# Performance work log

Hardware: AMD Instinct MI355X
Metric: run time of the kernel (lower is better)

The kernel has to match this reference:

```python
import jax, jax.numpy as jnp
import numpy as np

B, H, W, C = 32, 56, 56, 512
NH, WS, SS = 16, 7, 3
HD = C // NH
N = WS * WS
HID = int(C * 4.0)
SCALE = HD ** -0.5
EPS = 1e-5


def _window_partition(x):
    # x: (B, H, W, C) -> (B*nW, WS, WS, C)
    b = x.shape[0]
    x = x.reshape(b, H // WS, WS, W // WS, WS, C)
    return x.transpose(0, 1, 3, 2, 4, 5).reshape(-1, WS, WS, C)


def _window_reverse(wins):
    b = wins.shape[0] // ((H // WS) * (W // WS))
    x = wins.reshape(b, H // WS, W // WS, WS, WS, C)
    return x.transpose(0, 1, 3, 2, 4, 5).reshape(b, H, W, C)


def _ln(x, g, b):
    mu = jnp.mean(x, -1, keepdims=True)
    var = jnp.mean((x - mu) ** 2, -1, keepdims=True)
    return (x - mu) * jax.lax.rsqrt(var + EPS) * g + b


def setup_inputs():
    key = jax.random.key(0)
    ks = jax.random.split(key, 8)

    def w(k, shape, s=0.02):
        return jax.random.normal(k, shape, jnp.float32) * s

    # relative position index (static, same recipe as Swin)
    coords = np.stack(np.meshgrid(np.arange(WS), np.arange(WS), indexing='ij'))  # (2,WS,WS)
    cf = coords.reshape(2, -1)
    rel = (cf[:, :, None] - cf[:, None, :]).transpose(1, 2, 0).astype(np.int64)
    rel[:, :, 0] += WS - 1
    rel[:, :, 1] += WS - 1
    rel[:, :, 0] *= 2 * WS - 1
    rel_index = jnp.asarray(rel.sum(-1), jnp.int32)  # (N, N)

    # shifted-window attention mask (static)
    img = np.zeros((H, W), np.float32)
    cnt = 0
    for hs in (slice(0, -WS), slice(-WS, -SS), slice(-SS, None)):
        for vs in (slice(0, -WS), slice(-WS, -SS), slice(-SS, None)):
            img[hs, vs] = cnt
            cnt += 1
    mw = img.reshape(H // WS, WS, W // WS, WS).transpose(0, 2, 1, 3).reshape(-1, N)
    am = mw[:, None, :] - mw[:, :, None]
    attn_mask = jnp.asarray(np.where(am != 0, -100.0, 0.0).astype(np.float32))  # (nW, N, N)

    return {
        'x': jax.random.normal(ks[0], (B, H * W, C), jnp.float32),
        'norm1_g': jnp.ones((C,), jnp.float32), 'norm1_b': jnp.zeros((C,), jnp.float32),
        'qkv_w': w(ks[1], (C, 3 * C)), 'qkv_b': jnp.zeros((3 * C,), jnp.float32),
        'rel_bias_table': w(ks[2], ((2 * WS - 1) ** 2, NH)),
        'proj_w': w(ks[3], (C, C)), 'proj_b': jnp.zeros((C,), jnp.float32),
        'norm2_g': jnp.ones((C,), jnp.float32), 'norm2_b': jnp.zeros((C,), jnp.float32),
        'fc1_w': w(ks[4], (C, HID)), 'fc1_b': jnp.zeros((HID,), jnp.float32),
        'fc2_w': w(ks[5], (HID, C)), 'fc2_b': jnp.zeros((C,), jnp.float32),
        'rel_index': rel_index,
        'attn_mask': attn_mask,
    }


def reference(x, norm1_g, norm1_b, qkv_w, qkv_b, rel_bias_table, proj_w, proj_b,
              norm2_g, norm2_b, fc1_w, fc1_b, fc2_w, fc2_b, rel_index, attn_mask):
    shortcut = x
    h = _ln(x, norm1_g, norm1_b).reshape(B, H, W, C)
    # cyclic shift (shift_size > 0 -> SW-MSA)
    h = jnp.roll(h, shift=(-SS, -SS), axis=(1, 2))
    wins = _window_partition(h).reshape(-1, N, C)  # (B*nW, N, C)
    Bn = wins.shape[0]

    qkv = (wins @ qkv_w + qkv_b).reshape(Bn, N, 3, NH, HD).transpose(2, 0, 3, 1, 4)
    q, k, v = qkv[0] * SCALE, qkv[1], qkv[2]  # (Bn, NH, N, HD)
    attn = jnp.einsum('bhnd,bhmd->bhnm', q, k)  # (Bn, NH, N, N)

    bias = rel_bias_table[rel_index.reshape(-1)].reshape(N, N, NH).transpose(2, 0, 1)
    attn = attn + bias[None]

    nW = attn_mask.shape[0]
    attn = attn.reshape(Bn // nW, nW, NH, N, N) + attn_mask[None, :, None]
    attn = jax.nn.softmax(attn.reshape(Bn, NH, N, N), axis=-1)

    o = jnp.einsum('bhnm,bhmd->bhnd', attn, v).transpose(0, 2, 1, 3).reshape(Bn, N, C)
    o = o @ proj_w + proj_b

    h = _window_reverse(o.reshape(-1, WS, WS, C))
    h = jnp.roll(h, shift=(SS, SS), axis=(1, 2)).reshape(B, H * W, C)
    x = shortcut + h

    m = _ln(x, norm2_g, norm2_b)
    m = jax.nn.gelu(m @ fc1_w + fc1_b, approximate=False) @ fc2_w + fc2_b
    return x + m
```

## Files before the change

kernel.cpp:

```cpp
#include <hip/hip_runtime.h>
#include <hip/hip_bf16.h>


typedef unsigned short u16;
typedef __bf16 bf16x8 __attribute__((ext_vector_type(8)));
typedef float floatx4 __attribute__((ext_vector_type(4)));

#define MROWS 100352
#define SCALE_ATTN 0.17677669529663687f

__device__ __forceinline__ float b2f(u16 u) {
    union { unsigned int i; float f; } c; c.i = ((unsigned int)u) << 16; return c.f;
}
__device__ __forceinline__ u16 f2b(float f) {
    union { float f; unsigned int u; } c; c.f = f;
    unsigned int r = c.u + 0x7fffu + ((c.u >> 16) & 1u);
    return (u16)(r >> 16);
}

__device__ __forceinline__ int win_token(int win, int n) {
    int b  = win >> 6;
    int wi = (win & 63) >> 3;
    int wj = win & 7;
    int ti = n / 7;
    int tj = n - ti * 7;
    int ii = wi * 7 + ti + 3; if (ii >= 56) ii -= 56;
    int jj = wj * 7 + tj + 3; if (jj >= 56) jj -= 56;
    return b * 3136 + ii * 56 + jj;
}

__global__ void detect_flag(const unsigned int* __restrict__ g1, int* __restrict__ flag) {
    if (threadIdx.x == 0 && blockIdx.x == 0)
        *flag = (g1[0] == 0x3F800000u) ? 1 : 0;
}

__global__ __launch_bounds__(256)
void conv_f32(const void* __restrict__ src, float* __restrict__ dst, int n,
              const int* __restrict__ flag) {
    int i = blockIdx.x * 256 + threadIdx.x;
    if (i >= n) return;
    if (*flag) dst[i] = ((const float*)src)[i];
    else       dst[i] = b2f(((const u16*)src)[i]);
}

__global__ __launch_bounds__(256)
void transpose_k(const void* __restrict__ srcv, u16* __restrict__ dst, int R, int Cc,
                 const int* __restrict__ flag) {
    const bool f32 = (*flag != 0);
    __shared__ u16 tile[32][33];
    int tx = threadIdx.x & 31, ty = threadIdx.x >> 5;
    int c0 = blockIdx.x << 5, r0 = blockIdx.y << 5;
#pragma unroll
    for (int j = 0; j < 4; ++j) {
        size_t idx = (size_t)(r0 + ty + j * 8) * Cc + c0 + tx;
        tile[ty + j * 8][tx] = f32 ? f2b(((const float*)srcv)[idx]) : ((const u16*)srcv)[idx];
    }
    __syncthreads();
#pragma unroll
    for (int j = 0; j < 4; ++j)
        dst[(size_t)(c0 + ty + j * 8) * R + r0 + tx] = tile[tx][ty + j * 8];
}

__global__ __launch_bounds__(256)
void bias_expand(const float* __restrict__ tblf, const int* __restrict__ ridx,
                 float* __restrict__ biasf) {
    int i = blockIdx.x * 256 + threadIdx.x;
    if (i < 16 * 2401) {
        int head = i / 2401, r = i - head * 2401;
        biasf[i] = tblf[ridx[r] * 16 + head];
    }
}

template <bool REMAP>
__global__ __launch_bounds__(256)
void ln_kernel(const void* __restrict__ srcv, const float* __restrict__ g,
               const float* __restrict__ bb, u16* __restrict__ dst,
               const int* __restrict__ flag) {
    int row = blockIdx.x;
    size_t srow;
    if (REMAP) {
        int win = row / 49, n = row - win * 49;
        srow = (size_t)win_token(win, n);
    } else {
        srow = (size_t)row;
    }
    int t = threadIdx.x;
    float v0, v1;
    if (REMAP && *flag) {
        float2 u = *(const float2*)((const float*)srcv + srow * 512 + t * 2);
        v0 = u.x; v1 = u.y;
    } else {
        ushort2 u = *(const ushort2*)((const u16*)srcv + srow * 512 + t * 2);
        v0 = b2f(u.x); v1 = b2f(u.y);
    }
    float sum = v0 + v1, sq = v0 * v0 + v1 * v1;
#pragma unroll
    for (int off = 32; off > 0; off >>= 1) {
        sum += __shfl_down(sum, off);
        sq  += __shfl_down(sq, off);
    }
    __shared__ float s1[4], s2[4];
    int wv = t >> 6, ln = t & 63;
    if (ln == 0) { s1[wv] = sum; s2[wv] = sq; }
    __syncthreads();
    float tot  = s1[0] + s1[1] + s1[2] + s1[3];
    float tot2 = s2[0] + s2[1] + s2[2] + s2[3];
    float mean = tot * (1.0f / 512.0f);
    float var  = tot2 * (1.0f / 512.0f) - mean * mean;
    float rstd = rsqrtf(var + 1e-5f);
    float o0 = (v0 - mean) * rstd * g[t * 2]     + bb[t * 2];
    float o1 = (v1 - mean) * rstd * g[t * 2 + 1] + bb[t * 2 + 1];
    ushort2 ou; ou.x = f2b(o0); ou.y = f2b(o1);
    *(ushort2*)(dst + (size_t)row * 512 + t * 2) = ou;
}

template <int MODE>
__global__ __launch_bounds__(256)
void gemm128(const u16* __restrict__ A, const u16* __restrict__ Bt,
             const float* __restrict__ bias, int K, int Nn,
             void* __restrict__ outv, const void* __restrict__ resv,
             const int* __restrict__ flag, int row_off) {
    __shared__ __align__(16) u16 As[128 * 40];
    __shared__ __align__(16) u16 Bs[128 * 40];
    const int tid = threadIdx.x;
    const int bm = blockIdx.x, bn = blockIdx.y;
    const int wave = tid >> 6, lane = tid & 63;
    const int wr = (wave >> 1) << 6, wc = (wave & 1) << 6;
    const int lm = lane & 15, lq = lane >> 4;
    const bool f32 = (*flag != 0);

    floatx4 acc[4][4];
#pragma unroll
    for (int i = 0; i < 4; ++i)
#pragma unroll
        for (int j = 0; j < 4; ++j)
            acc[i][j] = (floatx4){0.f, 0.f, 0.f, 0.f};

    const size_t arow0 = (size_t)bm * 128;
    const size_t brow0 = (size_t)bn * 128;

    for (int k0 = 0; k0 < K; k0 += 32) {
#pragma unroll
        for (int it = 0; it < 2; ++it) {
            int chunk = tid + (it << 8);
            int r = chunk >> 2;
            int kc = (chunk & 3) << 3;
            uint4 da = *(const uint4*)(A  + (arow0 + r) * K + k0 + kc);
            uint4 db = *(const uint4*)(Bt + (brow0 + r) * K + k0 + kc);
            *(uint4*)(&As[r * 40 + kc]) = da;
            *(uint4*)(&Bs[r * 40 + kc]) = db;
        }
        __syncthreads();
        bf16x8 af[4], bf[4];
#pragma unroll
        for (int i = 0; i < 4; ++i)
            af[i] = *(const bf16x8*)(&As[(wr + (i << 4) + lm) * 40 + (lq << 3)]);
#pragma unroll
        for (int j = 0; j < 4; ++j)
            bf[j] = *(const bf16x8*)(&Bs[(wc + (j << 4) + lm) * 40 + (lq << 3)]);
#pragma unroll
        for (int i = 0; i < 4; ++i)
#pragma unroll
            for (int j = 0; j < 4; ++j)
                acc[i][j] = __builtin_amdgcn_mfma_f32_16x16x32_bf16(af[i], bf[j], acc[i][j], 0, 0, 0);
        __syncthreads();
    }

#pragma unroll
    for (int i = 0; i < 4; ++i) {
#pragma unroll
        for (int r = 0; r < 4; ++r) {
            const int row = (bm << 7) + wr + (i << 4) + (lq << 2) + r;
            size_t orow;
            if (MODE == 2) {
                int win = row / 49, n = row - win * 49;
                orow = (size_t)win_token(win, n);
            } else {
                orow = (size_t)row;
            }
#pragma unroll
            for (int j = 0; j < 4; ++j) {
                const int col = (bn << 7) + wc + (j << 4) + lm;
                float v = acc[i][j][r] + bias[col];
                if (MODE == 0) {
                    ((u16*)outv)[(size_t)row * Nn + col] = f2b(v);
                } else if (MODE == 1) {
                    v = 0.5f * v * (1.0f + erff(v * 0.70710678118654752f));
                    ((u16*)outv)[(size_t)row * Nn + col] = f2b(v);
                } else if (MODE == 2) {
                    float res = f32 ? ((const float*)resv)[orow * 512 + col]
                                    : b2f(((const u16*)resv)[orow * 512 + col]);
                    ((u16*)outv)[orow * 512 + col] = f2b(v + res);
                } else {
                    float res = b2f(((const u16*)resv)[(size_t)row * Nn + col]);
                    size_t grow = (size_t)(row + row_off);
                    if (f32) ((float*)outv)[grow * Nn + col] = v + res;
                    else     ((u16*)outv)[grow * Nn + col]  = f2b(v + res);
                }
            }
        }
    }
}

__global__ __launch_bounds__(64)
void attn_kernel(const u16* __restrict__ qkv, const float* __restrict__ biasf,
                 const float* __restrict__ amaskf, u16* __restrict__ o, int win_base) {
    const int blk = blockIdx.x;
    const int winl = blk >> 4, head = blk & 15;
    const int wing = win_base + winl;
    const int w = wing & 63;
    const int t = threadIdx.x;
    __shared__ float qf[49 * 32], kf[49 * 32], vf[49 * 32];
    const size_t base = (size_t)winl * 49 * 1536 + head * 32;
    for (int idx = t; idx < 392; idx += 64) {
        int m = idx >> 3, d = (idx & 7) << 2;
        size_t rb = base + (size_t)m * 1536 + d;
        ushort4 uq = *(const ushort4*)(qkv + rb);
        ushort4 uk = *(const ushort4*)(qkv + rb + 512);
        ushort4 uv = *(const ushort4*)(qkv + rb + 1024);
        int o4 = m * 32 + d;
        qf[o4 + 0] = b2f(uq.x); qf[o4 + 1] = b2f(uq.y);
        qf[o4 + 2] = b2f(uq.z); qf[o4 + 3] = b2f(uq.w);
        kf[o4 + 0] = b2f(uk.x); kf[o4 + 1] = b2f(uk.y);
        kf[o4 + 2] = b2f(uk.z); kf[o4 + 3] = b2f(uk.w);
        vf[o4 + 0] = b2f(uv.x); vf[o4 + 1] = b2f(uv.y);
        vf[o4 + 2] = b2f(uv.z); vf[o4 + 3] = b2f(uv.w);
    }
    __syncthreads();
    if (t < 49) {
        float q[32];
#pragma unroll
        for (int d = 0; d < 32; ++d) q[d] = qf[t * 32 + d] * SCALE_ATTN;
        float s[49];
        float mx = -1e30f;
        const float* bp = biasf + head * 2401 + t * 49;
        const float* mp = amaskf + w * 2401 + t * 49;
#pragma unroll
        for (int m = 0; m < 49; ++m) {
            float acc = 0.f;
#pragma unroll
            for (int d = 0; d < 32; ++d) acc += q[d] * kf[m * 32 + d];
            acc += bp[m] + mp[m];
            s[m] = acc;
            mx = fmaxf(mx, acc);
        }
        float sum = 0.f;
#pragma unroll
        for (int m = 0; m < 49; ++m) { s[m] = __expf(s[m] - mx); sum += s[m]; }
        float inv = 1.0f / sum;
        float ov[32];
#pragma unroll
        for (int d = 0; d < 32; ++d) ov[d] = 0.f;
#pragma unroll
        for (int m = 0; m < 49; ++m) {
            float p = s[m];
#pragma unroll
            for (int d = 0; d < 32; ++d) ov[d] += p * vf[m * 32 + d];
        }
        u16* op = o + (size_t)(wing * 49 + t) * 512 + head * 32;
#pragma unroll
        for (int dc = 0; dc < 32; dc += 4) {
            ushort4 pk;
            pk.x = f2b(ov[dc + 0] * inv); pk.y = f2b(ov[dc + 1] * inv);
            pk.z = f2b(ov[dc + 2] * inv); pk.w = f2b(ov[dc + 3] * inv);
            *(ushort4*)(op + dc) = pk;
        }
    }
}

extern "C" void kernel_launch(void* const* d_in, const int* in_sizes, int n_in,
                              void* d_out, int out_size, void* d_ws, size_t ws_size,
                              hipStream_t stream) {
    const void* x      = d_in[0];
    const void* n1g    = d_in[1];
    const void* n1b    = d_in[2];
    const void* qkv_w  = d_in[3];
    const void* qkv_b  = d_in[4];
    const void* relt   = d_in[5];
    const void* proj_w = d_in[6];
    const void* proj_b = d_in[7];
    const void* n2g    = d_in[8];
    const void* n2b    = d_in[9];
    const void* fc1_w  = d_in[10];
    const void* fc1_b  = d_in[11];
    const void* fc2_w  = d_in[12];
    const void* fc2_b  = d_in[13];
    const int*  ridx   = (const int*)d_in[14];
    const void* amask  = d_in[15];

    char* ws = (char*)d_ws;
    u16*  wT_qkv  = (u16*)(ws);
    u16*  wT_proj = (u16*)(ws + 1572864);
    u16*  wT_fc1  = (u16*)(ws + 2097152);
    u16*  wT_fc2  = (u16*)(ws + 4194304);
    float* biasf  = (float*)(ws + 6291456);
    float* amaskf = (float*)(ws + 6445120);
    float* qkv_bf = (float*)(ws + 7059776);
    float* proj_bf= (float*)(ws + 7065920);
    float* fc1_bf = (float*)(ws + 7067968);
    float* fc2_bf = (float*)(ws + 7076160);
    float* n1gf   = (float*)(ws + 7078208);
    float* n1bf   = (float*)(ws + 7080256);
    float* n2gf   = (float*)(ws + 7082304);
    float* n2bf   = (float*)(ws + 7084352);
    float* reltf  = (float*)(ws + 7086400);
    int*   flag   = (int*)(ws + 7097216);
    u16* bufA = (u16*)(ws + 8388608);
    u16* bufB = (u16*)(ws + 8388608 + 102760448);
    u16* bufC = (u16*)(ws + 8388608 + 102760448 + 77070336);

    detect_flag<<<1, 64, 0, stream>>>((const unsigned int*)n1g, flag);

    conv_f32<<<6, 256, 0, stream>>>(qkv_b, qkv_bf, 1536, flag);
    conv_f32<<<2, 256, 0, stream>>>(proj_b, proj_bf, 512, flag);
    conv_f32<<<8, 256, 0, stream>>>(fc1_b, fc1_bf, 2048, flag);
    conv_f32<<<2, 256, 0, stream>>>(fc2_b, fc2_bf, 512, flag);
    conv_f32<<<2, 256, 0, stream>>>(n1g, n1gf, 512, flag);
    conv_f32<<<2, 256, 0, stream>>>(n1b, n1bf, 512, flag);
    conv_f32<<<2, 256, 0, stream>>>(n2g, n2gf, 512, flag);
    conv_f32<<<2, 256, 0, stream>>>(n2b, n2bf, 512, flag);
    conv_f32<<<11, 256, 0, stream>>>(relt, reltf, 169 * 16, flag);
    conv_f32<<<(64 * 2401 + 255) / 256, 256, 0, stream>>>(amask, amaskf, 64 * 2401, flag);

    transpose_k<<<dim3(48, 16), 256, 0, stream>>>(qkv_w, wT_qkv, 512, 1536, flag);
    transpose_k<<<dim3(16, 16), 256, 0, stream>>>(proj_w, wT_proj, 512, 512, flag);
    transpose_k<<<dim3(64, 16), 256, 0, stream>>>(fc1_w, wT_fc1, 512, 2048, flag);
    transpose_k<<<dim3(16, 64), 256, 0, stream>>>(fc2_w, wT_fc2, 2048, 512, flag);
    bias_expand<<<(16 * 2401 + 255) / 256, 256, 0, stream>>>(reltf, ridx, biasf);

    ln_kernel<true><<<MROWS, 256, 0, stream>>>(x, n1gf, n1bf, bufA, flag);

    for (int c = 0; c < 4; ++c) {
        const u16* Ain = bufA + (size_t)c * 25088 * 512;
        gemm128<0><<<dim3(196, 12), 256, 0, stream>>>(Ain, wT_qkv, qkv_bf, 512, 1536, bufB, nullptr, flag, 0);
        attn_kernel<<<512 * 16, 64, 0, stream>>>(bufB, biasf, amaskf, bufC, c * 512);
    }

    gemm128<2><<<dim3(784, 4), 256, 0, stream>>>(bufC, wT_proj, proj_bf, 512, 512, bufA, x, flag, 0);

    ln_kernel<false><<<MROWS, 256, 0, stream>>>(bufA, n2gf, n2bf, bufC, flag);

    for (int mc0 = 0; mc0 < MROWS; mc0 += 16384) {
        int rows = (MROWS - mc0 < 16384) ? (MROWS - mc0) : 16384;
        int tiles = rows >> 7;
        gemm128<1><<<dim3(tiles, 16), 256, 0, stream>>>(bufC + (size_t)mc0 * 512, wT_fc1, fc1_bf, 512, 2048, bufB, nullptr, flag, 0);
        gemm128<3><<<dim3(tiles, 4), 256, 0, stream>>>(bufB, wT_fc2, fc2_bf, 2048, 512, d_out, bufA + (size_t)mc0 * 512, flag, mc0);
    }
}
```

Baseline: 2.418 ms.

## Rewrite GEMM as 256x256 tile with async global-to-LDS double buffering

Replaces the 128x128 register-staged GEMM with a 256x256, 512-thread kernel. It loads tiles directly into LDS via global_load_lds, double-buffered with explicit waitcnt/barrier pipelining, uses an XOR-swizzled LDS layout, and remaps workgroups across XCDs. The aim is to hide global load latency, cut LDS bank conflicts and raise data reuse per tile for all four GEMMs. The trade-off is much higher register and LDS pressure, plus tight reliance on hand-placed wait counts for correctness. Row counts must also divide evenly by 256.

```diff
diff --git a/kernel.cpp b/kernel.cpp
--- a/kernel.cpp
+++ b/kernel.cpp
@@ -28,6 +28,11 @@
     int jj = wj * 7 + tj + 3; if (jj >= 56) jj -= 56;
     return b * 3136 + ii * 56 + jj;
 }
+
+#define GL2LDS(gaddr, laddr) \
+    __builtin_amdgcn_global_load_lds((const __attribute__((address_space(1))) void*)(gaddr), \
+                                     (__attribute__((address_space(3))) void*)(laddr), 16, 0, 0)
+#define SCHED0() __builtin_amdgcn_sched_barrier(0)
 
 __global__ void detect_flag(const unsigned int* __restrict__ g1, int* __restrict__ flag) {
     if (threadIdx.x == 0 && blockIdx.x == 0)
@@ -115,62 +120,113 @@
 }
 
 template <int MODE>
-__global__ __launch_bounds__(256)
-void gemm128(const u16* __restrict__ A, const u16* __restrict__ Bt,
-             const float* __restrict__ bias, int K, int Nn,
+__global__ __launch_bounds__(512, 2)
+void gemm256(const u16* __restrict__ A, const u16* __restrict__ Bt,
+             const float* __restrict__ bias, int K, int Nn, int nbn,
              void* __restrict__ outv, const void* __restrict__ resv,
              const int* __restrict__ flag, int row_off) {
-    __shared__ __align__(16) u16 As[128 * 40];
-    __shared__ __align__(16) u16 Bs[128 * 40];
+    __shared__ __align__(16) u16 As[2 * 16384];
+    __shared__ __align__(16) u16 Bs[2 * 16384];
     const int tid = threadIdx.x;
-    const int bm = blockIdx.x, bn = blockIdx.y;
+
+    const int nwg = (int)gridDim.x;
+    const int bid = (int)blockIdx.x;
+    const int q8 = nwg >> 3, r8 = nwg & 7;
+    const int xcd = bid & 7, sidx = bid >> 3;
+    const int xb = (xcd < r8) ? xcd * (q8 + 1) : r8 * (q8 + 1) + (xcd - r8) * q8;
+    const int wg = xb + sidx;
+    const int bm = wg / nbn, bn = wg - bm * nbn;
+
     const int wave = tid >> 6, lane = tid & 63;
-    const int wr = (wave >> 1) << 6, wc = (wave & 1) << 6;
+    const int wm = wave >> 2, wn = wave & 3;
     const int lm = lane & 15, lq = lane >> 4;
-    const bool f32 = (*flag != 0);
-
-    floatx4 acc[4][4];
-#pragma unroll
-    for (int i = 0; i < 4; ++i)
+    const int lm7 = lm & 7;
+
+    floatx4 acc[8][4];
+#pragma unroll
+    for (int i = 0; i < 8; ++i)
 #pragma unroll
         for (int j = 0; j < 4; ++j)
             acc[i][j] = (floatx4){0.f, 0.f, 0.f, 0.f};
 
-    const size_t arow0 = (size_t)bm * 128;
-    const size_t brow0 = (size_t)bn * 128;
-
-    for (int k0 = 0; k0 < K; k0 += 32) {
-#pragma unroll
-        for (int it = 0; it < 2; ++it) {
-            int chunk = tid + (it << 8);
-            int r = chunk >> 2;
-            int kc = (chunk & 3) << 3;
-            uint4 da = *(const uint4*)(A  + (arow0 + r) * K + k0 + kc);
-            uint4 db = *(const uint4*)(Bt + (brow0 + r) * K + k0 + kc);
-            *(uint4*)(&As[r * 40 + kc]) = da;
-            *(uint4*)(&Bs[r * 40 + kc]) = db;
+    const size_t arow0 = (size_t)bm * 256;
+    const size_t brow0 = (size_t)bn * 256;
+
+    const int crow = lane >> 3;
+    const int csl  = ((lane & 7) ^ crow) << 3;
+    const u16* gA[4]; const u16* gB[4]; int lofs[4];
+#pragma unroll
+    for (int qq = 0; qq < 4; ++qq) {
+        const int c = (wave << 2) + qq;
+        gA[qq] = A  + (arow0 + c * 8 + crow) * (size_t)K + csl;
+        gB[qq] = Bt + (brow0 + c * 8 + crow) * (size_t)K + csl;
+        lofs[qq] = c << 9;
+    }
+    const int NT = K >> 6;
+
+    auto STAGE = [&](int buf, int kt) {
+        const size_t ko = (size_t)kt << 6;
+        const int lb_ = buf << 14;
+#pragma unroll
+        for (int qq = 0; qq < 4; ++qq) {
+            GL2LDS(gA[qq] + ko, &As[lb_ + lofs[qq]]);
+            GL2LDS(gB[qq] + ko, &Bs[lb_ + lofs[qq]]);
         }
-        __syncthreads();
-        bf16x8 af[4], bf[4];
-#pragma unroll
-        for (int i = 0; i < 4; ++i)
-            af[i] = *(const bf16x8*)(&As[(wr + (i << 4) + lm) * 40 + (lq << 3)]);
+    };
+
+    STAGE(0, 0);
+    STAGE(1, 1);
+    SCHED0();
+    asm volatile("s_waitcnt vmcnt(8)" ::: "memory");
+    SCHED0();
+    __builtin_amdgcn_s_barrier();
+    SCHED0();
+
+    for (int t = 0; t < NT; ++t) {
+        const int lb = (t & 1) << 14;
+        bf16x8 af[8], bfv[4];
+#pragma unroll
+        for (int i = 0; i < 8; ++i)
+            af[i] = *(const bf16x8*)(&As[lb + ((wm << 7) + (i << 4) + lm) * 64 + ((lq ^ lm7) << 3)]);
 #pragma unroll
         for (int j = 0; j < 4; ++j)
-            bf[j] = *(const bf16x8*)(&Bs[(wc + (j << 4) + lm) * 40 + (lq << 3)]);
-#pragma unroll
-        for (int i = 0; i < 4; ++i)
+            bfv[j] = *(const bf16x8*)(&Bs[lb + ((wn << 6) + (j << 4) + lm) * 64 + ((lq ^ lm7) << 3)]);
+#pragma unroll
+        for (int i = 0; i < 8; ++i)
 #pragma unroll
             for (int j = 0; j < 4; ++j)
-                acc[i][j] = __builtin_amdgcn_mfma_f32_16x16x32_bf16(af[i], bf[j], acc[i][j], 0, 0, 0);
-        __syncthreads();
-    }
-
-#pragma unroll
-    for (int i = 0; i < 4; ++i) {
-#pragma unroll
-        for (int r = 0; r < 4; ++r) {
-            const int row = (bm << 7) + wr + (i << 4) + (lq << 2) + r;
+                acc[i][j] = __builtin_amdgcn_mfma_f32_16x16x32_bf16(af[i], bfv[j], acc[i][j], 0, 0, 0);
+#pragma unroll
+        for (int i = 0; i < 8; ++i)
+            af[i] = *(const bf16x8*)(&As[lb + ((wm << 7) + (i << 4) + lm) * 64 + (((4 + lq) ^ lm7) << 3)]);
+#pragma unroll
+        for (int j = 0; j < 4; ++j)
+            bfv[j] = *(const bf16x8*)(&Bs[lb + ((wn << 6) + (j << 4) + lm) * 64 + (((4 + lq) ^ lm7) << 3)]);
+        asm volatile("s_waitcnt lgkmcnt(0)" ::: "memory");
+        SCHED0();
+        __builtin_amdgcn_s_barrier();
+        SCHED0();
+        if (t + 2 < NT) STAGE(t & 1, t + 2);
+        SCHED0();
+#pragma unroll
+        for (int i = 0; i < 8; ++i)
+#pragma unroll
+            for (int j = 0; j < 4; ++j)
+                acc[i][j] = __builtin_amdgcn_mfma_f32_16x16x32_bf16(af[i], bfv[j], acc[i][j], 0, 0, 0);
+        SCHED0();
+        if (t + 2 < NT) asm volatile("s_waitcnt vmcnt(8)" ::: "memory");
+        else            asm volatile("s_waitcnt vmcnt(0)" ::: "memory");
+        SCHED0();
+        __builtin_amdgcn_s_barrier();
+        SCHED0();
+    }
+
+    const bool f32 = (MODE >= 2) ? (*flag != 0) : false;
+#pragma unroll
+    for (int i = 0; i < 8; ++i) {
+#pragma unroll
+        for (int rr = 0; rr < 4; ++rr) {
+            const int row = (bm << 8) + (wm << 7) + (i << 4) + (lq << 2) + rr;
             size_t orow;
             if (MODE == 2) {
                 int win = row / 49, n = row - win * 49;
@@ -180,8 +236,8 @@
             }
 #pragma unroll
             for (int j = 0; j < 4; ++j) {
-                const int col = (bn << 7) + wc + (j << 4) + lm;
-                float v = acc[i][j][r] + bias[col];
+                const int col = (bn << 8) + (wn << 6) + (j << 4) + lm;
+                float v = acc[i][j][rr] + bias[col];
                 if (MODE == 0) {
                     ((u16*)outv)[(size_t)row * Nn + col] = f2b(v);
                 } else if (MODE == 1) {
@@ -332,18 +388,18 @@
 
     for (int c = 0; c < 4; ++c) {
         const u16* Ain = bufA + (size_t)c * 25088 * 512;
-        gemm128<0><<<dim3(196, 12), 256, 0, stream>>>(Ain, wT_qkv, qkv_bf, 512, 1536, bufB, nullptr, flag, 0);
+        gemm256<0><<<98 * 6, 512, 0, stream>>>(Ain, wT_qkv, qkv_bf, 512, 1536, 6, bufB, nullptr, flag, 0);
         attn_kernel<<<512 * 16, 64, 0, stream>>>(bufB, biasf, amaskf, bufC, c * 512);
     }
 
-    gemm128<2><<<dim3(784, 4), 256, 0, stream>>>(bufC, wT_proj, proj_bf, 512, 512, bufA, x, flag, 0);
+    gemm256<2><<<392 * 2, 512, 0, stream>>>(bufC, wT_proj, proj_bf, 512, 512, 2, bufA, x, flag, 0);
 
     ln_kernel<false><<<MROWS, 256, 0, stream>>>(bufA, n2gf, n2bf, bufC, flag);
 
     for (int mc0 = 0; mc0 < MROWS; mc0 += 16384) {
         int rows = (MROWS - mc0 < 16384) ? (MROWS - mc0) : 16384;
-        int tiles = rows >> 7;
-        gemm128<1><<<dim3(tiles, 16), 256, 0, stream>>>(bufC + (size_t)mc0 * 512, wT_fc1, fc1_bf, 512, 2048, bufB, nullptr, flag, 0);
-        gemm128<3><<<dim3(tiles, 4), 256, 0, stream>>>(bufB, wT_fc2, fc2_bf, 2048, 512, d_out, bufA + (size_t)mc0 * 512, flag, mc0);
-    }
-}
+        int tiles = rows >> 8;
+        gemm256<1><<<tiles * 8, 512, 0, stream>>>(bufC + (size_t)mc0 * 512, wT_fc1, fc1_bf, 512, 2048, 8, bufB, nullptr, flag, 0);
+        gemm256<3><<<tiles * 2, 512, 0, stream>>>(bufB, wT_fc2, fc2_bf, 2048, 512, 2, d_out, bufA + (size_t)mc0 * 512, flag, mc0);
+    }
+}
```

Result: slower. 2.553 ms (+5.6%).
